# Kernel tuning notes

Measured on AMD Instinct MI355X. Metric: run time of the kernel, lower is better.

Reference implementation:

```python
import jax, jax.numpy as jnp
import numpy as np


def setup_inputs() -> dict:
    key = jax.random.key(0)
    k1, k2, k3 = jax.random.split(key, 3)
    x = jax.random.normal(k1, (16, 128, 128, 64), dtype=jnp.float32)
    kernel = jax.random.normal(k2, (3, 3, 64, 128), dtype=jnp.float32) * 0.05
    bias = jax.random.normal(k3, (128,), dtype=jnp.float32) * 0.05
    return {"x": x, "kernel": kernel, "bias": bias}


def reference(x, kernel, bias):
    # Faithful to myconv2d: extract_patches (stride 1, rate 1, SAME) followed by
    # per-out-channel multiply+reduce over the flattened (kh*kw*cin) patch axis,
    # which is mathematically a stride-1 SAME conv2d. Expressed as a direct conv.
    out = jax.lax.conv_general_dilated(
        x, kernel,
        window_strides=(1, 1),
        padding="SAME",
        dimension_numbers=("NHWC", "HWIO", "NHWC"),
    )
    return out + bias  # bias broadcast over channel dim, as in call()
```

## Files before the change

kernel.cpp:

```cpp
#include <hip/hip_runtime.h>


#define HH 128
#define WW 128
#define CIN 64
#define COUT 128

typedef __attribute__((ext_vector_type(8))) short v8s;
typedef __attribute__((ext_vector_type(4))) float v4f;

#define ROW_CHUNKS 1040
#define WS_NEEDED  (9u * CIN * COUT * 2u)

static __device__ __forceinline__ unsigned short f2bf(float f) {
    unsigned int u = __float_as_uint(f);
    unsigned int r = (u + 0x7fffu + ((u >> 16) & 1u)) >> 16;
    return (unsigned short)r;
}

__global__ __launch_bounds__(256) void cvt_w(const float* __restrict__ wgt,
                                             unsigned short* __restrict__ wt) {
    int idx = blockIdx.x * 256 + threadIdx.x;
    if (idx >= 9 * CIN * COUT) return;
    int co  = idx & (COUT - 1);
    int ci  = (idx >> 7) & (CIN - 1);
    int tap = idx >> 13;
    wt[(tap * COUT + co) * CIN + ci] = f2bf(wgt[idx]);
}

__global__ __launch_bounds__(256, 3) void conv_mfma(
    const float* __restrict__ x,
    const unsigned short* __restrict__ wt,
    const float* __restrict__ bias,
    float* __restrict__ out) {
    __shared__ v8s smem[3 * ROW_CHUNKS];

    int bid = blockIdx.x;
    int logical = ((bid & 7) << 8) | (bid >> 3);
    int h = logical & (HH - 1);
    int n = logical >> 7;

    int tid  = threadIdx.x;
    int lane = tid & 63;
    int wid  = tid >> 6;
    int wi = wid >> 1;
    int wj = wid & 1;
    int l15  = lane & 15;
    int quad = lane >> 4;
    int pixelL = wi * 64 + l15;

    if (tid < 48) {
        int row = tid >> 4, k = tid & 15;
        int c = (k < 8) ? k : (1024 + k);
        smem[row * ROW_CHUNKS + c] = (v8s)(short)0;
    }

    #pragma unroll
    for (int dh = 0; dh < 3; ++dh) {
        int ih = h + dh - 1;
        if (ih < 0 || ih >= HH) continue;
        const float* rowf = x + ((size_t)(n * HH + ih)) * WW * CIN;
        #pragma unroll
        for (int k = 0; k < 4; ++k) {
            int c = 8 + tid + (k << 8);
            const float* p = rowf + (size_t)(c - 8) * 8;
            float4 a = *(const float4*)p;
            float4 b = *(const float4*)(p + 4);
            v8s ch;
            ch[0] = (short)f2bf(a.x); ch[1] = (short)f2bf(a.y);
            ch[2] = (short)f2bf(a.z); ch[3] = (short)f2bf(a.w);
            ch[4] = (short)f2bf(b.x); ch[5] = (short)f2bf(b.y);
            ch[6] = (short)f2bf(b.z); ch[7] = (short)f2bf(b.w);
            int cp = c ^ ((c >> 3) & 7);
            smem[dh * ROW_CHUNKS + cp] = ch;
        }
    }
    __syncthreads();

    v4f acc[4][4];
    #pragma unroll
    for (int i = 0; i < 4; ++i)
        #pragma unroll
        for (int j = 0; j < 4; ++j) acc[i][j] = (v4f)0.f;

    #pragma unroll
    for (int dh = 0; dh < 3; ++dh) {
        int ih = h + dh - 1;
        if (ih < 0 || ih >= HH) continue;
        const v8s* srow = smem + dh * ROW_CHUNKS;
        #pragma unroll
        for (int dw = 0; dw < 3; ++dw) {
            const unsigned short* wtap = wt + (dh * 3 + dw) * COUT * CIN;
            #pragma unroll
            for (int kc = 0; kc < 2; ++kc) {
                v8s bfrag[4];
                #pragma unroll
                for (int t = 0; t < 4; ++t) {
                    int co = wj * 64 + t * 16 + l15;
                    bfrag[t] = *(const v8s*)(wtap + co * CIN + kc * 32 + quad * 8);
                }
                v8s afrag[4];
                #pragma unroll
                for (int t = 0; t < 4; ++t) {
                    int pl = pixelL + t * 16 + dw;
                    int c  = pl * 8 + kc * 4 + quad;
                    afrag[t] = srow[c ^ (pl & 7)];
                }
                #pragma unroll
                for (int ti = 0; ti < 4; ++ti)
                    #pragma unroll
                    for (int tj = 0; tj < 4; ++tj)
                        acc[ti][tj] = __builtin_amdgcn_mfma_f32_16x16x32_bf16(
                            afrag[ti], bfrag[tj], acc[ti][tj], 0, 0, 0);
            }
        }
    }

    float bv[4];
    #pragma unroll
    for (int tj = 0; tj < 4; ++tj) bv[tj] = bias[wj * 64 + tj * 16 + l15];

    float* orow = out + ((size_t)(n * HH + h)) * WW * COUT;
    #pragma unroll
    for (int ti = 0; ti < 4; ++ti) {
        #pragma unroll
        for (int r = 0; r < 4; ++r) {
            int p = wi * 64 + ti * 16 + quad * 4 + r;
            float* op = orow + (size_t)p * COUT + wj * 64 + l15;
            #pragma unroll
            for (int tj = 0; tj < 4; ++tj)
                op[tj * 16] = acc[ti][tj][r] + bv[tj];
        }
    }
}

__global__ __launch_bounds__(256) void conv3x3_direct(
    const float* __restrict__ x, const float* __restrict__ wgt,
    const float* __restrict__ bias, float* __restrict__ out) {
    int idx = blockIdx.x * 256 + threadIdx.x;
    int co = idx & (COUT - 1);
    int w  = (idx >> 7) & (WW - 1);
    int h  = (idx >> 14) & (HH - 1);
    int n  = idx >> 21;
    float acc = bias[co];
    #pragma unroll
    for (int kh = 0; kh < 3; ++kh) {
        int ih = h + kh - 1;
        if (ih < 0 || ih >= HH) continue;
        #pragma unroll
        for (int kw = 0; kw < 3; ++kw) {
            int iw = w + kw - 1;
            if (iw < 0 || iw >= WW) continue;
            const float* xp = x + (((size_t)(n * HH + ih) * WW + iw) * CIN);
            const float* wp = wgt + ((size_t)((kh * 3 + kw) * CIN)) * COUT + co;
            #pragma unroll 8
            for (int ci = 0; ci < CIN; ++ci)
                acc = fmaf(xp[ci], wp[(size_t)ci * COUT], acc);
        }
    }
    out[idx] = acc;
}

extern "C" void kernel_launch(void* const* d_in, const int* in_sizes, int n_in,
                              void* d_out, int out_size, void* d_ws, size_t ws_size,
                              hipStream_t stream) {
    const float* x    = (const float*)d_in[0];
    const float* wgt  = (const float*)d_in[1];
    const float* bias = (const float*)d_in[2];
    float* out = (float*)d_out;

    if (ws_size < (size_t)WS_NEEDED) {
        int blocks = (out_size + 255) / 256;
        conv3x3_direct<<<blocks, 256, 0, stream>>>(x, wgt, bias, out);
        return;
    }

    unsigned short* wt = (unsigned short*)d_ws;
    cvt_w<<<(9 * CIN * COUT + 255) / 256, 256, 0, stream>>>(wgt, wt);
    conv_mfma<<<16 * HH, 256, 0, stream>>>(x, wt, bias, out);
}
```

Baseline: 256.0 us.

## Process four output rows per block with rolling smem row buffer and prefetch

New measurement: 301.6 us. 17.8% more time.

```diff
diff --git a/kernel.cpp b/kernel.cpp
--- a/kernel.cpp
+++ b/kernel.cpp
@@ -5,6 +5,7 @@
 #define WW 128
 #define CIN 64
 #define COUT 128
+#define HS 4
 
 typedef __attribute__((ext_vector_type(8))) short v8s;
 typedef __attribute__((ext_vector_type(4))) float v4f;
@@ -28,17 +29,18 @@
     wt[(tap * COUT + co) * CIN + ci] = f2bf(wgt[idx]);
 }
 
-__global__ __launch_bounds__(256, 3) void conv_mfma(
+__global__ __launch_bounds__(256, 2) void conv_mfma(
     const float* __restrict__ x,
     const unsigned short* __restrict__ wt,
     const float* __restrict__ bias,
     float* __restrict__ out) {
-    __shared__ v8s smem[3 * ROW_CHUNKS];
+    __shared__ v8s smem[4 * ROW_CHUNKS];
 
     int bid = blockIdx.x;
-    int logical = ((bid & 7) << 8) | (bid >> 3);
-    int h = logical & (HH - 1);
-    int n = logical >> 7;
+    int logical = ((bid & 7) << 6) | (bid >> 3);
+    int hg = logical & 31;
+    int n  = logical >> 5;
+    int h0 = hg * HS;
 
     int tid  = threadIdx.x;
     int lane = tid & 63;
@@ -49,87 +51,143 @@
     int quad = lane >> 4;
     int pixelL = wi * 64 + l15;
 
-    if (tid < 48) {
-        int row = tid >> 4, k = tid & 15;
+    const float* xn = x + (size_t)n * HH * WW * CIN;
+
+    if (tid < 64) {
+        int slot = tid >> 4, k = tid & 15;
         int c = (k < 8) ? k : (1024 + k);
-        smem[row * ROW_CHUNKS + c] = (v8s)(short)0;
+        smem[slot * ROW_CHUNKS + c] = (v8s)(short)0;
     }
 
     #pragma unroll
-    for (int dh = 0; dh < 3; ++dh) {
-        int ih = h + dh - 1;
-        if (ih < 0 || ih >= HH) continue;
-        const float* rowf = x + ((size_t)(n * HH + ih)) * WW * CIN;
-        #pragma unroll
-        for (int k = 0; k < 4; ++k) {
-            int c = 8 + tid + (k << 8);
-            const float* p = rowf + (size_t)(c - 8) * 8;
-            float4 a = *(const float4*)p;
-            float4 b = *(const float4*)(p + 4);
-            v8s ch;
-            ch[0] = (short)f2bf(a.x); ch[1] = (short)f2bf(a.y);
-            ch[2] = (short)f2bf(a.z); ch[3] = (short)f2bf(a.w);
-            ch[4] = (short)f2bf(b.x); ch[5] = (short)f2bf(b.y);
-            ch[6] = (short)f2bf(b.z); ch[7] = (short)f2bf(b.w);
-            int cp = c ^ ((c >> 3) & 7);
-            smem[dh * ROW_CHUNKS + cp] = ch;
+    for (int s = 0; s < 3; ++s) {
+        int ih = h0 + s - 1;
+        v8s* dst = smem + s * ROW_CHUNKS;
+        if (ih >= 0) {
+            const float* rowf = xn + (size_t)ih * WW * CIN;
+            #pragma unroll
+            for (int k = 0; k < 4; ++k) {
+                int c = 8 + tid + (k << 8);
+                const float* p = rowf + (size_t)(c - 8) * 8;
+                float4 a = *(const float4*)p;
+                float4 b = *(const float4*)(p + 4);
+                v8s ch;
+                ch[0] = (short)f2bf(a.x); ch[1] = (short)f2bf(a.y);
+                ch[2] = (short)f2bf(a.z); ch[3] = (short)f2bf(a.w);
+                ch[4] = (short)f2bf(b.x); ch[5] = (short)f2bf(b.y);
+                ch[6] = (short)f2bf(b.z); ch[7] = (short)f2bf(b.w);
+                dst[c ^ ((c >> 3) & 7)] = ch;
+            }
+        } else {
+            #pragma unroll
+            for (int k = 0; k < 4; ++k) {
+                int c = 8 + tid + (k << 8);
+                dst[c ^ ((c >> 3) & 7)] = (v8s)(short)0;
+            }
         }
     }
     __syncthreads();
-
-    v4f acc[4][4];
-    #pragma unroll
-    for (int i = 0; i < 4; ++i)
-        #pragma unroll
-        for (int j = 0; j < 4; ++j) acc[i][j] = (v4f)0.f;
-
-    #pragma unroll
-    for (int dh = 0; dh < 3; ++dh) {
-        int ih = h + dh - 1;
-        if (ih < 0 || ih >= HH) continue;
-        const v8s* srow = smem + dh * ROW_CHUNKS;
-        #pragma unroll
-        for (int dw = 0; dw < 3; ++dw) {
-            const unsigned short* wtap = wt + (dh * 3 + dw) * COUT * CIN;
-            #pragma unroll
-            for (int kc = 0; kc < 2; ++kc) {
-                v8s bfrag[4];
-                #pragma unroll
-                for (int t = 0; t < 4; ++t) {
-                    int co = wj * 64 + t * 16 + l15;
-                    bfrag[t] = *(const v8s*)(wtap + co * CIN + kc * 32 + quad * 8);
-                }
-                v8s afrag[4];
-                #pragma unroll
-                for (int t = 0; t < 4; ++t) {
-                    int pl = pixelL + t * 16 + dw;
-                    int c  = pl * 8 + kc * 4 + quad;
-                    afrag[t] = srow[c ^ (pl & 7)];
-                }
-                #pragma unroll
-                for (int ti = 0; ti < 4; ++ti)
-                    #pragma unroll
-                    for (int tj = 0; tj < 4; ++tj)
-                        acc[ti][tj] = __builtin_amdgcn_mfma_f32_16x16x32_bf16(
-                            afrag[ti], bfrag[tj], acc[ti][tj], 0, 0, 0);
-            }
-        }
-    }
 
     float bv[4];
     #pragma unroll
     for (int tj = 0; tj < 4; ++tj) bv[tj] = bias[wj * 64 + tj * 16 + l15];
 
-    float* orow = out + ((size_t)(n * HH + h)) * WW * COUT;
-    #pragma unroll
-    for (int ti = 0; ti < 4; ++ti) {
-        #pragma unroll
-        for (int r = 0; r < 4; ++r) {
-            int p = wi * 64 + ti * 16 + quad * 4 + r;
-            float* op = orow + (size_t)p * COUT + wj * 64 + l15;
-            #pragma unroll
-            for (int tj = 0; tj < 4; ++tj)
-                op[tj * 16] = acc[ti][tj][r] + bv[tj];
+    #pragma unroll 1
+    for (int t = 0; t < HS; ++t) {
+        bool last = (t == HS - 1);
+        int ihn = h0 + t + 2;
+        bool inr = (ihn < HH);
+
+        float4 nxt[8];
+        if (!last && inr) {
+            const float* rowf = xn + (size_t)ihn * WW * CIN;
+            #pragma unroll
+            for (int k = 0; k < 4; ++k) {
+                const float* p = rowf + (size_t)(tid + (k << 8)) * 8;
+                nxt[2 * k]     = *(const float4*)p;
+                nxt[2 * k + 1] = *(const float4*)(p + 4);
+            }
+        }
+
+        v4f acc[4][4];
+        #pragma unroll
+        for (int i = 0; i < 4; ++i)
+            #pragma unroll
+            for (int j = 0; j < 4; ++j) acc[i][j] = (v4f)0.f;
+
+        #pragma unroll
+        for (int dh = 0; dh < 3; ++dh) {
+            const v8s* srow = smem + ((t + dh) & 3) * ROW_CHUNKS;
+            #pragma unroll
+            for (int dw = 0; dw < 3; ++dw) {
+                const unsigned short* wtap = wt + (dh * 3 + dw) * COUT * CIN;
+                #pragma unroll
+                for (int kc = 0; kc < 2; ++kc) {
+                    v8s bfrag[4];
+                    #pragma unroll
+                    for (int tt = 0; tt < 4; ++tt) {
+                        int co = wj * 64 + tt * 16 + l15;
+                        bfrag[tt] = *(const v8s*)(wtap + co * CIN + kc * 32 + quad * 8);
+                    }
+                    v8s afrag[4];
+                    #pragma unroll
+                    for (int tt = 0; tt < 4; ++tt) {
+                        int pl = pixelL + tt * 16 + dw;
+                        int c  = pl * 8 + kc * 4 + quad;
+                        afrag[tt] = srow[c ^ (pl & 7)];
+                    }
+                    #pragma unroll
+                    for (int ti = 0; ti < 4; ++ti)
+                        #pragma unroll
+                        for (int tj = 0; tj < 4; ++tj)
+                            acc[ti][tj] = __builtin_amdgcn_mfma_f32_16x16x32_bf16(
+                                afrag[ti], bfrag[tj], acc[ti][tj], 0, 0, 0);
+                }
+            }
+        }
+
+        if (!last) {
+            asm volatile("s_waitcnt vmcnt(0)" ::: "memory");
+            v8s* dst = smem + ((t + 3) & 3) * ROW_CHUNKS;
+            if (inr) {
+                #pragma unroll
+                for (int k = 0; k < 4; ++k) {
+                    int c = 8 + tid + (k << 8);
+                    float4 a = nxt[2 * k], b = nxt[2 * k + 1];
+                    v8s ch;
+                    ch[0] = (short)f2bf(a.x); ch[1] = (short)f2bf(a.y);
+                    ch[2] = (short)f2bf(a.z); ch[3] = (short)f2bf(a.w);
+                    ch[4] = (short)f2bf(b.x); ch[5] = (short)f2bf(b.y);
+                    ch[6] = (short)f2bf(b.z); ch[7] = (short)f2bf(b.w);
+                    dst[c ^ ((c >> 3) & 7)] = ch;
+                }
+            } else {
+                #pragma unroll
+                for (int k = 0; k < 4; ++k) {
+                    int c = 8 + tid + (k << 8);
+                    dst[c ^ ((c >> 3) & 7)] = (v8s)(short)0;
+                }
+            }
+        }
+
+        float* orow = out + ((size_t)(n * HH + (h0 + t))) * WW * COUT;
+        #pragma unroll
+        for (int ti = 0; ti < 4; ++ti) {
+            #pragma unroll
+            for (int r = 0; r < 4; ++r) {
+                int p = wi * 64 + ti * 16 + quad * 4 + r;
+                float* op = orow + (size_t)p * COUT + wj * 64 + l15;
+                #pragma unroll
+                for (int tj = 0; tj < 4; ++tj)
+                    op[tj * 16] = acc[ti][tj][r] + bv[tj];
+            }
+        }
+
+        if (!last) {
+            asm volatile("s_waitcnt lgkmcnt(0)" ::: "memory");
+            __builtin_amdgcn_sched_barrier(0);
+            __builtin_amdgcn_s_barrier();
+            __builtin_amdgcn_sched_barrier(0);
         }
     }
 }
@@ -177,5 +235,5 @@
 
     unsigned short* wt = (unsigned short*)d_ws;
     cvt_w<<<(9 * CIN * COUT + 255) / 256, 256, 0, stream>>>(wgt, wt);
-    conv_mfma<<<16 * HH, 256, 0, stream>>>(x, wt, bias, out);
-}
+    conv_mfma<<<16 * HH / HS, 256, 0, stream>>>(x, wt, bias, out);
+}
```

## Pre-convert input to bf16 in workspace and read MFMA fragments directly from global

Applied to the files above, without the earlier changes.

New measurement: 340.4 us. 33.0% more time.

```diff
diff --git a/kernel.cpp b/kernel.cpp
--- a/kernel.cpp
+++ b/kernel.cpp
@@ -10,7 +10,8 @@
 typedef __attribute__((ext_vector_type(4))) float v4f;
 
 #define ROW_CHUNKS 1040
-#define WS_NEEDED  (9u * CIN * COUT * 2u)
+#define WS_WT     (9u * CIN * COUT * 2u)
+#define WS_FULL   (WS_WT + 16u * HH * WW * CIN * 2u)
 
 static __device__ __forceinline__ unsigned short f2bf(float f) {
     unsigned int u = __float_as_uint(f);
@@ -28,7 +29,102 @@
     wt[(tap * COUT + co) * CIN + ci] = f2bf(wgt[idx]);
 }
 
-__global__ __launch_bounds__(256, 3) void conv_mfma(
+__global__ __launch_bounds__(256) void cvt_x(const float* __restrict__ x,
+                                             unsigned short* __restrict__ xb) {
+    size_t idx = (size_t)blockIdx.x * 256 + threadIdx.x;
+    const float4* xp = (const float4*)x;
+    float4 a = xp[2 * idx];
+    float4 b = xp[2 * idx + 1];
+    v8s ch;
+    ch[0] = (short)f2bf(a.x); ch[1] = (short)f2bf(a.y);
+    ch[2] = (short)f2bf(a.z); ch[3] = (short)f2bf(a.w);
+    ch[4] = (short)f2bf(b.x); ch[5] = (short)f2bf(b.y);
+    ch[6] = (short)f2bf(b.z); ch[7] = (short)f2bf(b.w);
+    ((v8s*)xb)[idx] = ch;
+}
+
+__global__ __launch_bounds__(256, 3) void conv_mfma_direct(
+    const unsigned short* __restrict__ xb,
+    const unsigned short* __restrict__ wt,
+    const float* __restrict__ bias,
+    float* __restrict__ out) {
+    int bid = blockIdx.x;
+    int logical = ((bid & 7) << 8) | (bid >> 3);
+    int h = logical & (HH - 1);
+    int n = logical >> 7;
+
+    int tid  = threadIdx.x;
+    int lane = tid & 63;
+    int wid  = tid >> 6;
+    int wi = wid >> 1;
+    int wj = wid & 1;
+    int l15  = lane & 15;
+    int quad = lane >> 4;
+    int pixelL = wi * 64 + l15;
+
+    v4f acc[4][4];
+    #pragma unroll
+    for (int i = 0; i < 4; ++i)
+        #pragma unroll
+        for (int j = 0; j < 4; ++j) acc[i][j] = (v4f)0.f;
+
+    #pragma unroll
+    for (int dh = 0; dh < 3; ++dh) {
+        int ih = h + dh - 1;
+        if (ih < 0 || ih >= HH) continue;
+        const unsigned short* rp = xb + ((size_t)(n * HH + ih)) * WW * CIN;
+        #pragma unroll
+        for (int dw = 0; dw < 3; ++dw) {
+            const unsigned short* wtap = wt + (dh * 3 + dw) * COUT * CIN;
+            #pragma unroll
+            for (int kc = 0; kc < 2; ++kc) {
+                v8s bfrag[4];
+                #pragma unroll
+                for (int tt = 0; tt < 4; ++tt) {
+                    int co = wj * 64 + tt * 16 + l15;
+                    bfrag[tt] = *(const v8s*)(wtap + co * CIN + kc * 32 + quad * 8);
+                }
+                v8s afrag[4];
+                #pragma unroll
+                for (int tt = 0; tt < 4; ++tt) {
+                    int pl = pixelL + tt * 16 + dw;
+                    const v8s* ap = (const v8s*)(rp + (size_t)(pl - 1) * CIN +
+                                                 kc * 32 + quad * 8);
+                    if ((tt == 0 && dw == 0) || (tt == 3 && dw == 2)) {
+                        afrag[tt] = (pl >= 1 && pl <= 128) ? *ap : (v8s)(short)0;
+                    } else {
+                        afrag[tt] = *ap;
+                    }
+                }
+                #pragma unroll
+                for (int ti = 0; ti < 4; ++ti)
+                    #pragma unroll
+                    for (int tj = 0; tj < 4; ++tj)
+                        acc[ti][tj] = __builtin_amdgcn_mfma_f32_16x16x32_bf16(
+                            afrag[ti], bfrag[tj], acc[ti][tj], 0, 0, 0);
+            }
+        }
+    }
+
+    float bv[4];
+    #pragma unroll
+    for (int tj = 0; tj < 4; ++tj) bv[tj] = bias[wj * 64 + tj * 16 + l15];
+
+    float* orow = out + ((size_t)(n * HH + h)) * WW * COUT;
+    #pragma unroll
+    for (int ti = 0; ti < 4; ++ti) {
+        #pragma unroll
+        for (int r = 0; r < 4; ++r) {
+            int p = wi * 64 + ti * 16 + quad * 4 + r;
+            float* op = orow + (size_t)p * COUT + wj * 64 + l15;
+            #pragma unroll
+            for (int tj = 0; tj < 4; ++tj)
+                op[tj * 16] = acc[ti][tj][r] + bv[tj];
+        }
+    }
+}
+
+__global__ __launch_bounds__(256, 3) void conv_mfma_lds(
     const float* __restrict__ x,
     const unsigned short* __restrict__ wt,
     const float* __restrict__ bias,
@@ -95,16 +191,16 @@
             for (int kc = 0; kc < 2; ++kc) {
                 v8s bfrag[4];
                 #pragma unroll
-                for (int t = 0; t < 4; ++t) {
-                    int co = wj * 64 + t * 16 + l15;
-                    bfrag[t] = *(const v8s*)(wtap + co * CIN + kc * 32 + quad * 8);
+                for (int tt = 0; tt < 4; ++tt) {
+                    int co = wj * 64 + tt * 16 + l15;
+                    bfrag[tt] = *(const v8s*)(wtap + co * CIN + kc * 32 + quad * 8);
                 }
                 v8s afrag[4];
                 #pragma unroll
-                for (int t = 0; t < 4; ++t) {
-                    int pl = pixelL + t * 16 + dw;
+                for (int tt = 0; tt < 4; ++tt) {
+                    int pl = pixelL + tt * 16 + dw;
                     int c  = pl * 8 + kc * 4 + quad;
-                    afrag[t] = srow[c ^ (pl & 7)];
+                    afrag[tt] = srow[c ^ (pl & 7)];
                 }
                 #pragma unroll
                 for (int ti = 0; ti < 4; ++ti)
@@ -169,7 +265,7 @@
     const float* bias = (const float*)d_in[2];
     float* out = (float*)d_out;
 
-    if (ws_size < (size_t)WS_NEEDED) {
+    if (ws_size < (size_t)WS_WT) {
         int blocks = (out_size + 255) / 256;
         conv3x3_direct<<<blocks, 256, 0, stream>>>(x, wgt, bias, out);
         return;
@@ -177,5 +273,13 @@
 
     unsigned short* wt = (unsigned short*)d_ws;
     cvt_w<<<(9 * CIN * COUT + 255) / 256, 256, 0, stream>>>(wgt, wt);
-    conv_mfma<<<16 * HH, 256, 0, stream>>>(x, wt, bias, out);
-}
+
+    if (ws_size >= (size_t)WS_FULL) {
+        unsigned short* xbuf = wt + 9 * CIN * COUT;
+        int nelem8 = 16 * HH * WW * CIN / 8;
+        cvt_x<<<nelem8 / 256, 256, 0, stream>>>(x, xbuf);
+        conv_mfma_direct<<<16 * HH, 256, 0, stream>>>(xbuf, wt, bias, out);
+    } else {
+        conv_mfma_lds<<<16 * HH, 256, 0, stream>>>(x, wt, bias, out);
+    }
+}
```

## Compute two output rows per block sharing a four-row input tile

Applied to the files above, without the earlier changes.

Result: slower. 266.2 us (+4.0%).

```diff
diff --git a/kernel.cpp b/kernel.cpp
--- a/kernel.cpp
+++ b/kernel.cpp
@@ -28,51 +28,61 @@
     wt[(tap * COUT + co) * CIN + ci] = f2bf(wgt[idx]);
 }
 
-__global__ __launch_bounds__(256, 3) void conv_mfma(
+__global__ __launch_bounds__(512, 4) void conv_mfma(
     const float* __restrict__ x,
     const unsigned short* __restrict__ wt,
     const float* __restrict__ bias,
     float* __restrict__ out) {
-    __shared__ v8s smem[3 * ROW_CHUNKS];
+    __shared__ v8s smem[4 * ROW_CHUNKS];
 
     int bid = blockIdx.x;
-    int logical = ((bid & 7) << 8) | (bid >> 3);
-    int h = logical & (HH - 1);
-    int n = logical >> 7;
+    int logical = ((bid & 7) << 7) | (bid >> 3);
+    int hg = logical & 63;
+    int n  = logical >> 6;
+    int h0 = hg * 2;
 
     int tid  = threadIdx.x;
     int lane = tid & 63;
     int wid  = tid >> 6;
-    int wi = wid >> 1;
-    int wj = wid & 1;
+    int rsel = wid >> 2;
+    int w2   = wid & 3;
+    int wi = w2 >> 1;
+    int wj = w2 & 1;
     int l15  = lane & 15;
     int quad = lane >> 4;
     int pixelL = wi * 64 + l15;
 
-    if (tid < 48) {
-        int row = tid >> 4, k = tid & 15;
+    if (tid < 64) {
+        int slot = tid >> 4, k = tid & 15;
         int c = (k < 8) ? k : (1024 + k);
-        smem[row * ROW_CHUNKS + c] = (v8s)(short)0;
+        smem[slot * ROW_CHUNKS + c] = (v8s)(short)0;
     }
 
     #pragma unroll
-    for (int dh = 0; dh < 3; ++dh) {
-        int ih = h + dh - 1;
-        if (ih < 0 || ih >= HH) continue;
-        const float* rowf = x + ((size_t)(n * HH + ih)) * WW * CIN;
-        #pragma unroll
-        for (int k = 0; k < 4; ++k) {
-            int c = 8 + tid + (k << 8);
-            const float* p = rowf + (size_t)(c - 8) * 8;
-            float4 a = *(const float4*)p;
-            float4 b = *(const float4*)(p + 4);
-            v8s ch;
-            ch[0] = (short)f2bf(a.x); ch[1] = (short)f2bf(a.y);
-            ch[2] = (short)f2bf(a.z); ch[3] = (short)f2bf(a.w);
-            ch[4] = (short)f2bf(b.x); ch[5] = (short)f2bf(b.y);
-            ch[6] = (short)f2bf(b.z); ch[7] = (short)f2bf(b.w);
-            int cp = c ^ ((c >> 3) & 7);
-            smem[dh * ROW_CHUNKS + cp] = ch;
+    for (int s = 0; s < 4; ++s) {
+        int ih = h0 + s - 1;
+        v8s* dst = smem + s * ROW_CHUNKS;
+        if (ih >= 0 && ih < HH) {
+            const float* rowf = x + ((size_t)(n * HH + ih)) * WW * CIN;
+            #pragma unroll
+            for (int k = 0; k < 2; ++k) {
+                int c = 8 + tid + (k << 9);
+                const float* p = rowf + (size_t)(c - 8) * 8;
+                float4 a = *(const float4*)p;
+                float4 b = *(const float4*)(p + 4);
+                v8s ch;
+                ch[0] = (short)f2bf(a.x); ch[1] = (short)f2bf(a.y);
+                ch[2] = (short)f2bf(a.z); ch[3] = (short)f2bf(a.w);
+                ch[4] = (short)f2bf(b.x); ch[5] = (short)f2bf(b.y);
+                ch[6] = (short)f2bf(b.z); ch[7] = (short)f2bf(b.w);
+                dst[c ^ ((c >> 3) & 7)] = ch;
+            }
+        } else {
+            #pragma unroll
+            for (int k = 0; k < 2; ++k) {
+                int c = 8 + tid + (k << 9);
+                dst[c ^ ((c >> 3) & 7)] = (v8s)(short)0;
+            }
         }
     }
     __syncthreads();
@@ -85,9 +95,7 @@
 
     #pragma unroll
     for (int dh = 0; dh < 3; ++dh) {
-        int ih = h + dh - 1;
-        if (ih < 0 || ih >= HH) continue;
-        const v8s* srow = smem + dh * ROW_CHUNKS;
+        const v8s* srow = smem + (rsel + dh) * ROW_CHUNKS;
         #pragma unroll
         for (int dw = 0; dw < 3; ++dw) {
             const unsigned short* wtap = wt + (dh * 3 + dw) * COUT * CIN;
@@ -95,16 +103,16 @@
             for (int kc = 0; kc < 2; ++kc) {
                 v8s bfrag[4];
                 #pragma unroll
-                for (int t = 0; t < 4; ++t) {
-                    int co = wj * 64 + t * 16 + l15;
-                    bfrag[t] = *(const v8s*)(wtap + co * CIN + kc * 32 + quad * 8);
+                for (int tt = 0; tt < 4; ++tt) {
+                    int co = wj * 64 + tt * 16 + l15;
+                    bfrag[tt] = *(const v8s*)(wtap + co * CIN + kc * 32 + quad * 8);
                 }
                 v8s afrag[4];
                 #pragma unroll
-                for (int t = 0; t < 4; ++t) {
-                    int pl = pixelL + t * 16 + dw;
+                for (int tt = 0; tt < 4; ++tt) {
+                    int pl = pixelL + tt * 16 + dw;
                     int c  = pl * 8 + kc * 4 + quad;
-                    afrag[t] = srow[c ^ (pl & 7)];
+                    afrag[tt] = srow[c ^ (pl & 7)];
                 }
                 #pragma unroll
                 for (int ti = 0; ti < 4; ++ti)
@@ -120,7 +128,7 @@
     #pragma unroll
     for (int tj = 0; tj < 4; ++tj) bv[tj] = bias[wj * 64 + tj * 16 + l15];
 
-    float* orow = out + ((size_t)(n * HH + h)) * WW * COUT;
+    float* orow = out + ((size_t)(n * HH + (h0 + rsel))) * WW * COUT;
     #pragma unroll
     for (int ti = 0; ti < 4; ++ti) {
         #pragma unroll
@@ -177,5 +185,5 @@
 
     unsigned short* wt = (unsigned short*)d_ws;
     cvt_w<<<(9 * CIN * COUT + 255) / 256, 256, 0, stream>>>(wgt, wt);
-    conv_mfma<<<16 * HH, 256, 0, stream>>>(x, wt, bias, out);
+    conv_mfma<<<16 * HH / 2, 512, 0, stream>>>(x, wt, bias, out);
 }
```
